# Kernel tuning notes

Hardware: AMD Instinct MI355X
Metric: run time of the kernel (lower is better)

The kernel has to match this reference:

```python
import jax, jax.numpy as jnp
import numpy as np

EPS = 1e-12  # matches torch F.normalize eps

def l2norm(x):
    n = jnp.linalg.norm(x, axis=-1, keepdims=True)
    return x / jnp.maximum(n, EPS)

def setup_inputs() -> dict:
    key = jax.random.key(0)
    ks = jax.random.split(key, 5)
    B, T, A, D, H = 32, 512, 64, 128, 256
    actions = jax.random.normal(ks[0], (B, T, A), dtype=jnp.float32)
    init_structure = jax.random.normal(ks[1], (D,), dtype=jnp.float32)
    # MLP params (scaled like typical init)
    w1 = jax.random.normal(ks[2], (A, H), dtype=jnp.float32) / jnp.sqrt(A)
    b1 = jnp.zeros((H,), dtype=jnp.float32)
    w2 = jax.random.normal(ks[3], (H, D * D), dtype=jnp.float32) / jnp.sqrt(H)
    b2 = jnp.zeros((D * D,), dtype=jnp.float32)
    return {"actions": actions, "init_structure": init_structure,
            "w1": w1, "b1": b1, "w2": w2, "b2": b2}

def reference(actions, init_structure, w1, b1, w2, b2):
    B, T, A = actions.shape
    D = init_structure.shape[0]
    # MLP: actions -> transition matrices [B, T, D, D]
    h = jax.nn.relu(jnp.einsum('bta,ah->bth', actions, w1) + b1)
    trans = (jnp.einsum('bth,hk->btk', h, w2) + b2).reshape(B, T, D, D)
    # initial structure, l2-normalized and broadcast over batch
    s0 = jnp.broadcast_to(l2norm(init_structure), (B, D))
    # sequential recurrence over time
    def step(s, Tm):  # s: [B, D], Tm: [B, D, D]
        s = jax.nn.relu(jnp.einsum('bi,bij->bj', s, Tm))
        s = l2norm(s)
        return s, s
    _, ys = jax.lax.scan(step, s0, jnp.swapaxes(trans, 0, 1))  # ys: [T, B, D]
    return jnp.swapaxes(ys, 0, 1)  # [B, T, D]
```

## Files before the change

kernel.cpp:

```cpp
#include <hip/hip_runtime.h>
#include <stdint.h>
#include <math.h>


typedef _Float16 f16x8 __attribute__((ext_vector_type(8)));
typedef float    f32x4 __attribute__((ext_vector_type(4)));

#define B_  32
#define T_  512
#define A_  64
#define H_  256
#define D_  128
#define N_  (D_ * D_)
#define M_  (B_ * T_)

__device__ inline void glds(const void* g, void* l) {
  __builtin_amdgcn_global_load_lds(
      (__attribute__((address_space(1))) void*)g,
      (__attribute__((address_space(3))) void*)l, 16, 0, 0);
}

__global__ __launch_bounds__(256) void w2cast_kernel(const float* __restrict__ w2,
                                                     _Float16* __restrict__ w2t) {
  __shared__ float tile[64][65];
  const int t = threadIdx.x;
  const int n0 = blockIdx.x * 64, k0 = blockIdx.y * 64;
  const int nn = t & 63, kg = t >> 6;
  #pragma unroll
  for (int r = 0; r < 16; ++r) {
    int k = kg * 16 + r;
    tile[k][nn] = w2[(size_t)(k0 + k) * N_ + n0 + nn];
  }
  __syncthreads();
  const int kk = t & 63, ng = t >> 6;
  #pragma unroll
  for (int r = 0; r < 16; ++r) {
    int n = ng * 16 + r;
    int ngl = n0 + n;
    int i = ngl >> 7, j = ngl & 127;
    int p = ((j >> 4) << 11) | ((i >> 5) << 9) | (((i >> 3) & 3) << 7)
          | ((j & 15) << 3) | (i & 7);
    w2t[(size_t)p * H_ + k0 + kk] = (_Float16)tile[kk][n];
  }
}

__global__ __launch_bounds__(256) void h_kernel(const float* __restrict__ actions,
                                                const float* __restrict__ w1,
                                                const float* __restrict__ b1,
                                                _Float16* __restrict__ h16) {
  __shared__ float w1s[32 * 256];
  __shared__ float acts[32 * 64];
  const int t = threadIdx.x;
  const size_t row0 = (size_t)blockIdx.x * 32;

  #pragma unroll
  for (int i = 0; i < 8; ++i) acts[t + i * 256] = actions[row0 * A_ + t + i * 256];

  float acc[32];
  float bj = b1[t];
  #pragma unroll
  for (int r = 0; r < 32; ++r) acc[r] = bj;

  for (int half = 0; half < 2; ++half) {
    __syncthreads();
    #pragma unroll
    for (int i = 0; i < 32; ++i) w1s[t + i * 256] = w1[half * 32 * 256 + t + i * 256];
    __syncthreads();
    #pragma unroll
    for (int r = 0; r < 32; ++r) {
      float a = acc[r];
      #pragma unroll
      for (int k = 0; k < 32; ++k)
        a += acts[r * 64 + half * 32 + k] * w1s[k * 256 + t];
      acc[r] = a;
    }
  }
  #pragma unroll
  for (int r = 0; r < 32; ++r)
    h16[(row0 + r) * H_ + t] = (_Float16)fmaxf(acc[r], 0.f);
}

__global__ __launch_bounds__(512, 2) void fused_kernel(
    const _Float16* __restrict__ h16, const _Float16* __restrict__ w2t,
    const float* __restrict__ b2, _Float16* __restrict__ tbuf0,
    _Float16* __restrict__ tbuf1, const float* __restrict__ init_s,
    float* __restrict__ out, float* __restrict__ dummyws,
    int Tc, int tcs, int c, int nch) {

  __shared__ __align__(16) char smem[49920];
  const int tid  = threadIdx.x;
  const int lane = tid & 63;
  const int w    = tid >> 6;

  if (blockIdx.x < 32) {
    if (c < 0) return;
    const char* trans = (const char*)((c & 1) ? tbuf1 : tbuf0);
    const int b  = blockIdx.x;
    const int t0 = c * Tc;
    const int n16 = lane & 15, q = lane >> 4;
    const int col = w * 16 + n16;
    float* red = (float*)(smem + 49664);
    _Float16* sb0p = (_Float16*)(smem + 49152);

    float v0 = 0.f;
    if (tid < 128) {
      v0 = (t0 == 0) ? init_s[tid] : out[((size_t)b * T_ + t0 - 1) * D_ + tid];
      float ss = v0 * v0;
      #pragma unroll
      for (int off = 32; off > 0; off >>= 1) ss += __shfl_xor(ss, off);
      if (lane == 0) red[w] = ss;
    }
    __syncthreads();
    if (tid < 128) {
      float inv0 = 1.f / fmaxf(sqrtf(red[0] + red[1]), 1e-12f);
      sb0p[tid] = (_Float16)(v0 * inv0);
    }
    __syncthreads();

    float uprev = (float)sb0p[col];

    const unsigned sbase = (unsigned)(size_t)(__attribute__((address_space(3))) char*)smem;
    const unsigned bq0 = sbase + w * 6144 + q * 256 + n16 * 16;
    const unsigned bq1 = bq0 + 3072;
    const unsigned aA0 = sbase + 49152 + q * 16;
    const unsigned aA1 = aA0 + 256;
    const unsigned aW0 = sbase + 49408 + col * 2;
    const unsigned aW1 = sbase + 49152 + col * 2;
    const char* Gw = trans + (size_t)b * Tc * 32768 + w * 4096 + lane * 16;
    float* outb = out + (size_t)b * T_ * D_ + col;
    float* dsink = dummyws + blockIdx.x * 128 + col;

    f16x8 r3[2];
    {
      const char* g0 = Gw;
      glds(g0,        smem + w * 6144);
      glds(g0 + 1024, smem + w * 6144 + 1024);
      glds(g0 + 2048, smem + w * 6144 + 2048);
      asm volatile("global_load_dwordx4 %0, %1, off"
                   : "=v"(r3[0]) : "v"(g0 + 3072) : "memory");
      const char* g1 = Gw + 32768;
      glds(g1,        smem + w * 6144 + 3072);
      glds(g1 + 1024, smem + w * 6144 + 3072 + 1024);
      glds(g1 + 2048, smem + w * 6144 + 3072 + 2048);
      asm volatile("global_load_dwordx4 %0, %1, off"
                   : "=v"(r3[1]) : "v"(g1 + 3072) : "memory");
    }

    const f32x4 zf = {0.f, 0.f, 0.f, 0.f};

#define STEP(TT, PAR, WAITN)                                                  \
    {                                                                         \
      const int tt = (TT);                                                    \
      f16x8 A0, A1, A2, A3, Bq0, Bq1, Bq2;                                    \
      asm volatile(                                                           \
        "s_waitcnt vmcnt(" #WAITN ")\n\t"                                     \
        "ds_read_b128 %0, %8 offset:0\n\t"                                    \
        "ds_read_b128 %1, %8 offset:64\n\t"                                   \
        "ds_read_b128 %2, %8 offset:128\n\t"                                  \
        "ds_read_b128 %3, %8 offset:192\n\t"                                  \
        "ds_read_b128 %4, %9 offset:0\n\t"                                    \
        "ds_read_b128 %5, %9 offset:1024\n\t"                                 \
        "ds_read_b128 %6, %9 offset:2048\n\t"                                 \
        "s_waitcnt lgkmcnt(0)"                                                \
        : "=v"(A0), "=v"(A1), "=v"(A2), "=v"(A3),                             \
          "=v"(Bq0), "=v"(Bq1), "=v"(Bq2), "+v"(r3[PAR])                      \
        : "v"(aA##PAR), "v"(bq##PAR) : "memory");                             \
      f32x4 c0 = __builtin_amdgcn_mfma_f32_16x16x32_f16(A0, Bq0, zf, 0, 0, 0);\
      f32x4 c1 = __builtin_amdgcn_mfma_f32_16x16x32_f16(A1, Bq1, zf, 0, 0, 0);\
      f32x4 c2 = __builtin_amdgcn_mfma_f32_16x16x32_f16(A2, Bq2, zf, 0, 0, 0);\
      f32x4 c3 = __builtin_amdgcn_mfma_f32_16x16x32_f16(A3, r3[PAR], zf, 0, 0, 0);\
      f32x4 cs = __builtin_amdgcn_mfma_f32_16x16x32_f16(A0, A0, zf, 0, 0, 0); \
      cs = __builtin_amdgcn_mfma_f32_16x16x32_f16(A1, A1, cs, 0, 0, 0);       \
      cs = __builtin_amdgcn_mfma_f32_16x16x32_f16(A2, A2, cs, 0, 0, 0);       \
      cs = __builtin_amdgcn_mfma_f32_16x16x32_f16(A3, A3, cs, 0, 0, 0);       \
      int nt = tt + 2; if (nt >= Tc) nt -= Tc;                                \
      const char* gd = Gw + (size_t)nt * 32768;                               \
      glds(gd,        smem + w * 6144 + (PAR) * 3072);                        \
      glds(gd + 1024, smem + w * 6144 + (PAR) * 3072 + 1024);                 \
      glds(gd + 2048, smem + w * 6144 + (PAR) * 3072 + 2048);                 \
      asm volatile("global_load_dwordx4 %0, %1, off"                          \
                   : "=v"(r3[PAR]) : "v"(gd + 3072) : "memory");              \
      float ssp = cs[0];                                                      \
      float inv = 1.f / fmaxf(sqrtf(ssp), 1e-12f);                            \
      float y = c0[0] + c1[0] + c2[0] + c3[0];                                \
      float un = fmaxf(y, 0.f) * inv;                                         \
      float o = uprev * inv;                                                  \
      uprev = un;                                                             \
      _Float16 hv = (_Float16)un;                                             \
      const int gt = t0 + tt;                                                 \
      float* gp = (gt > 0) ? (outb + (size_t)(gt - 1) * D_) : dsink;          \
      asm volatile("ds_write_b16 %0, %1\n\t"                                  \
                   "global_store_dword %2, %3, off"                           \
                   :: "v"(aW##PAR), "v"(hv), "v"(gp), "v"(o) : "memory");     \
      asm volatile("s_waitcnt lgkmcnt(0)\n\ts_barrier" ::: "memory");         \
    }

    STEP(0, 0, 4)
    STEP(1, 1, 5)
    for (int tt0 = 2; tt0 < Tc; tt0 += 2) {
      STEP(tt0, 0, 6)
      STEP(tt0 + 1, 1, 6)
    }
#undef STEP
    asm volatile("s_waitcnt vmcnt(0)" ::: "memory");

    {
      float x = 0.f;
      if (lane < 16) x = (float)((_Float16*)(smem + 49152))[col];
      float ss2 = x * x;
      ss2 += __shfl_xor(ss2, 1);
      ss2 += __shfl_xor(ss2, 2);
      ss2 += __shfl_xor(ss2, 4);
      ss2 += __shfl_xor(ss2, 8);
      if (lane == 0) red[w] = ss2;
      __syncthreads();
      float tot = 0.f;
      #pragma unroll
      for (int g = 0; g < 8; ++g) tot += red[g];
      float inv = 1.f / fmaxf(sqrtf(tot), 1e-12f);
      if (lane < 16) outb[(size_t)(t0 + Tc - 1) * D_] = uprev * inv;
    }
  } else {
    const int g = c + 1;
    if (g >= nch) return;
    _Float16* trans = (g & 1) ? tbuf1 : tbuf0;
    const int t0g = g * Tc;

    _Float16* smA = (_Float16*)smem;
    _Float16* smB = (_Float16*)(smem + 16384);

    const int wm = w >> 2, wn = w & 3;
    const int fm = lane & 15, fq = lane >> 4;
    const f32x4 zero = {0.f, 0.f, 0.f, 0.f};

    const int cA0 = tid, cA1 = tid + 512;
    const int rA0 = cA0 >> 2, kA0 = cA0 & 3;
    const int rA1 = cA1 >> 2, kA1 = cA1 & 3;

    const int mtiles = (B_ * Tc) >> 8;
    const int ntot = mtiles * 64;
    for (int tile = (int)blockIdx.x - 32; tile < ntot; tile += 224) {
      const int bn = tile & 63;
      const int bm = tile >> 6;

      const int mc0 = bm * 256 + rA0, mc1 = bm * 256 + rA1;
      const int bb0 = mc0 >> tcs, bb1 = mc1 >> tcs;
      const _Float16* gA0 = h16 + ((size_t)bb0 * T_ + t0g + (mc0 & (Tc - 1))) * H_ + kA0 * 8;
      const _Float16* gA1 = h16 + ((size_t)bb1 * T_ + t0g + (mc1 & (Tc - 1))) * H_ + kA1 * 8;
      const _Float16* gB0 = w2t + ((size_t)bn * 256 + rA0) * H_ + kA0 * 8;
      const _Float16* gB1 = w2t + ((size_t)bn * 256 + rA1) * H_ + kA1 * 8;
      _Float16* lA0 = &smA[cA0 * 8];
      _Float16* lA1 = &smA[cA1 * 8];
      _Float16* lB0 = &smB[cA0 * 8];
      _Float16* lB1 = &smB[cA1 * 8];

      f32x4 acc[8][4];
      #pragma unroll
      for (int i = 0; i < 8; ++i)
        #pragma unroll
        for (int j = 0; j < 4; ++j) acc[i][j] = zero;

      for (int kt = 0; kt < H_ / 32; ++kt) {
        __syncthreads();
        glds(gA0 + kt * 32, lA0);
        glds(gA1 + kt * 32, lA1);
        glds(gB0 + kt * 32, lB0);
        glds(gB1 + kt * 32, lB1);
        __syncthreads();
        f16x8 af[8], bf[4];
        #pragma unroll
        for (int mt = 0; mt < 8; ++mt)
          af[mt] = *(const f16x8*)&smA[(wm * 128 + mt * 16 + fm) * 32 + fq * 8];
        #pragma unroll
        for (int nt = 0; nt < 4; ++nt)
          bf[nt] = *(const f16x8*)&smB[(wn * 64 + nt * 16 + fm) * 32 + fq * 8];
        #pragma unroll
        for (int mt = 0; mt < 8; ++mt)
          #pragma unroll
          for (int nt = 0; nt < 4; ++nt)
            acc[mt][nt] = __builtin_amdgcn_mfma_f32_16x16x32_f16(af[mt], bf[nt], acc[mt][nt], 0, 0, 0);
      }

      #pragma unroll
      for (int nt = 0; nt < 4; ++nt) {
        int col = bn * 256 + wn * 64 + nt * 16 + fm;
        int pw = col >> 11, pf = (col >> 9) & 3, pq = (col >> 7) & 3;
        int pn = (col >> 3) & 15, pr = col & 7;
        int ii = pf * 32 + pq * 8 + pr, jj = pw * 16 + pn;
        float bias = b2[ii * 128 + jj];
        #pragma unroll
        for (int mt = 0; mt < 8; ++mt) {
          #pragma unroll
          for (int r = 0; r < 4; ++r) {
            long row = bm * 256 + wm * 128 + mt * 16 + fq * 4 + r;
            trans[row * (long)N_ + col] = (_Float16)(acc[mt][nt][r] + bias);
          }
        }
      }
      __syncthreads();
    }
  }
}

extern "C" void kernel_launch(void* const* d_in, const int* in_sizes, int n_in,
                              void* d_out, int out_size, void* d_ws, size_t ws_size,
                              hipStream_t stream) {
  const float* actions = (const float*)d_in[0];
  const float* init_s  = (const float*)d_in[1];
  const float* w1      = (const float*)d_in[2];
  const float* b1      = (const float*)d_in[3];
  const float* w2      = (const float*)d_in[4];
  const float* b2      = (const float*)d_in[5];
  float* out = (float*)d_out;

  uint8_t* ws = (uint8_t*)d_ws;
  _Float16* w2t = (_Float16*)ws;
  _Float16* h16 = (_Float16*)(ws + ((size_t)8 << 20));
  const size_t trans_off = (size_t)16 << 20;

  int Tc = 16;
  const int cands[3] = {64, 32, 16};
  for (int i = 0; i < 3; ++i) {
    if (trans_off + 2 * ((size_t)cands[i] << 20) + 65536 <= ws_size) { Tc = cands[i]; break; }
  }
  const int tcs = __builtin_ctz(Tc);
  _Float16* tbuf0 = (_Float16*)(ws + trans_off);
  _Float16* tbuf1 = (_Float16*)(ws + trans_off + ((size_t)Tc << 20));
  float* dummyws = (float*)(ws + trans_off + 2 * ((size_t)Tc << 20));

  w2cast_kernel<<<dim3(N_ / 64, 4), 256, 0, stream>>>(w2, w2t);
  h_kernel<<<M_ / 32, 256, 0, stream>>>(actions, w1, b1, h16);

  const int nch = T_ / Tc;
  for (int c = -1; c < nch; ++c) {
    fused_kernel<<<256, 512, 0, stream>>>(
        h16, w2t, b2, tbuf0, tbuf1, init_s, out, dummyws, Tc, tcs, c, nch);
  }
}
```

Measured before the change: 524.2 us.

## Stream transition tiles into a 4-deep register ring instead of LDS

The recurrence blocks now load each step's transition-matrix B fragments straight into registers with four global_load_dwordx4 per slot, keeping a ring four steps deep. Before, three of the four fragments went through LDS via global_load_lds in a two-deep buffer. This removes LDS staging and the ds_reads of B, lengthens prefetch distance to hide global latency, and shrinks shared memory. In exchange it uses many more VGPRs (16 f16x8 ring registers), which could spill under launch_bounds(512,2). The wraparound index now uses a mask, so Tc must be a power of two.

After: 522.7 us. Within noise of the previous version (-0.3%).

```diff
diff --git a/kernel.cpp b/kernel.cpp
--- a/kernel.cpp
+++ b/kernel.cpp
@@ -87,7 +87,7 @@
     float* __restrict__ out, float* __restrict__ dummyws,
     int Tc, int tcs, int c, int nch) {
 
-  __shared__ __align__(16) char smem[49920];
+  __shared__ __align__(16) char smem[33536];
   const int tid  = threadIdx.x;
   const int lane = tid & 63;
   const int w    = tid >> 6;
@@ -99,8 +99,9 @@
     const int t0 = c * Tc;
     const int n16 = lane & 15, q = lane >> 4;
     const int col = w * 16 + n16;
-    float* red = (float*)(smem + 49664);
-    _Float16* sb0p = (_Float16*)(smem + 49152);
+    const int Tcm1 = Tc - 1;
+    float* red = (float*)(smem + 33280);
+    _Float16* sb0p = (_Float16*)(smem + 32768);
 
     float v0 = 0.f;
     if (tid < 128) {
@@ -120,66 +121,55 @@
     float uprev = (float)sb0p[col];
 
     const unsigned sbase = (unsigned)(size_t)(__attribute__((address_space(3))) char*)smem;
-    const unsigned bq0 = sbase + w * 6144 + q * 256 + n16 * 16;
-    const unsigned bq1 = bq0 + 3072;
-    const unsigned aA0 = sbase + 49152 + q * 16;
-    const unsigned aA1 = aA0 + 256;
-    const unsigned aW0 = sbase + 49408 + col * 2;
-    const unsigned aW1 = sbase + 49152 + col * 2;
+    const unsigned aA0 = sbase + 32768 + q * 16;
+    const unsigned aA1 = sbase + 33024 + q * 16;
+    const unsigned aW0 = sbase + 33024 + col * 2;
+    const unsigned aW1 = sbase + 32768 + col * 2;
     const char* Gw = trans + (size_t)b * Tc * 32768 + w * 4096 + lane * 16;
     float* outb = out + (size_t)b * T_ * D_ + col;
     float* dsink = dummyws + blockIdx.x * 128 + col;
 
-    f16x8 r3[2];
-    {
-      const char* g0 = Gw;
-      glds(g0,        smem + w * 6144);
-      glds(g0 + 1024, smem + w * 6144 + 1024);
-      glds(g0 + 2048, smem + w * 6144 + 2048);
-      asm volatile("global_load_dwordx4 %0, %1, off"
-                   : "=v"(r3[0]) : "v"(g0 + 3072) : "memory");
-      const char* g1 = Gw + 32768;
-      glds(g1,        smem + w * 6144 + 3072);
-      glds(g1 + 1024, smem + w * 6144 + 3072 + 1024);
-      glds(g1 + 2048, smem + w * 6144 + 3072 + 2048);
-      asm volatile("global_load_dwordx4 %0, %1, off"
-                   : "=v"(r3[1]) : "v"(g1 + 3072) : "memory");
-    }
+    f16x8 ring[4][4];
+#define LDSLOT(S, P)                                                          \
+    asm volatile("global_load_dwordx4 %0, %4, off\n\t"                        \
+                 "global_load_dwordx4 %1, %4, off offset:1024\n\t"            \
+                 "global_load_dwordx4 %2, %4, off offset:2048\n\t"            \
+                 "global_load_dwordx4 %3, %4, off offset:3072"                \
+                 : "=v"(ring[S][0]), "=v"(ring[S][1]),                        \
+                   "=v"(ring[S][2]), "=v"(ring[S][3])                         \
+                 : "v"(P) : "memory")
+    LDSLOT(0, Gw + 0 * 32768);
+    LDSLOT(1, Gw + 1 * 32768);
+    LDSLOT(2, Gw + 2 * 32768);
+    LDSLOT(3, Gw + 3 * 32768);
 
     const f32x4 zf = {0.f, 0.f, 0.f, 0.f};
 
-#define STEP(TT, PAR, WAITN)                                                  \
+#define STEP(TT, PAR, SPAR, WAITN)                                            \
     {                                                                         \
       const int tt = (TT);                                                    \
-      f16x8 A0, A1, A2, A3, Bq0, Bq1, Bq2;                                    \
+      f16x8 A0, A1, A2, A3;                                                   \
       asm volatile(                                                           \
         "s_waitcnt vmcnt(" #WAITN ")\n\t"                                     \
         "ds_read_b128 %0, %8 offset:0\n\t"                                    \
         "ds_read_b128 %1, %8 offset:64\n\t"                                   \
         "ds_read_b128 %2, %8 offset:128\n\t"                                  \
         "ds_read_b128 %3, %8 offset:192\n\t"                                  \
-        "ds_read_b128 %4, %9 offset:0\n\t"                                    \
-        "ds_read_b128 %5, %9 offset:1024\n\t"                                 \
-        "ds_read_b128 %6, %9 offset:2048\n\t"                                 \
         "s_waitcnt lgkmcnt(0)"                                                \
         : "=v"(A0), "=v"(A1), "=v"(A2), "=v"(A3),                             \
-          "=v"(Bq0), "=v"(Bq1), "=v"(Bq2), "+v"(r3[PAR])                      \
-        : "v"(aA##PAR), "v"(bq##PAR) : "memory");                             \
-      f32x4 c0 = __builtin_amdgcn_mfma_f32_16x16x32_f16(A0, Bq0, zf, 0, 0, 0);\
-      f32x4 c1 = __builtin_amdgcn_mfma_f32_16x16x32_f16(A1, Bq1, zf, 0, 0, 0);\
-      f32x4 c2 = __builtin_amdgcn_mfma_f32_16x16x32_f16(A2, Bq2, zf, 0, 0, 0);\
-      f32x4 c3 = __builtin_amdgcn_mfma_f32_16x16x32_f16(A3, r3[PAR], zf, 0, 0, 0);\
+          "+v"(ring[PAR][0]), "+v"(ring[PAR][1]),                             \
+          "+v"(ring[PAR][2]), "+v"(ring[PAR][3])                              \
+        : "v"(aA##SPAR) : "memory");                                          \
+      f32x4 c0 = __builtin_amdgcn_mfma_f32_16x16x32_f16(A0, ring[PAR][0], zf, 0, 0, 0); \
+      f32x4 c1 = __builtin_amdgcn_mfma_f32_16x16x32_f16(A1, ring[PAR][1], zf, 0, 0, 0); \
+      f32x4 c2 = __builtin_amdgcn_mfma_f32_16x16x32_f16(A2, ring[PAR][2], zf, 0, 0, 0); \
+      f32x4 c3 = __builtin_amdgcn_mfma_f32_16x16x32_f16(A3, ring[PAR][3], zf, 0, 0, 0); \
       f32x4 cs = __builtin_amdgcn_mfma_f32_16x16x32_f16(A0, A0, zf, 0, 0, 0); \
       cs = __builtin_amdgcn_mfma_f32_16x16x32_f16(A1, A1, cs, 0, 0, 0);       \
       cs = __builtin_amdgcn_mfma_f32_16x16x32_f16(A2, A2, cs, 0, 0, 0);       \
       cs = __builtin_amdgcn_mfma_f32_16x16x32_f16(A3, A3, cs, 0, 0, 0);       \
-      int nt = tt + 2; if (nt >= Tc) nt -= Tc;                                \
-      const char* gd = Gw + (size_t)nt * 32768;                               \
-      glds(gd,        smem + w * 6144 + (PAR) * 3072);                        \
-      glds(gd + 1024, smem + w * 6144 + (PAR) * 3072 + 1024);                 \
-      glds(gd + 2048, smem + w * 6144 + (PAR) * 3072 + 2048);                 \
-      asm volatile("global_load_dwordx4 %0, %1, off"                          \
-                   : "=v"(r3[PAR]) : "v"(gd + 3072) : "memory");              \
+      const char* gd = Gw + (size_t)((tt + 4) & Tcm1) * 32768;                \
+      LDSLOT(PAR, gd);                                                        \
       float ssp = cs[0];                                                      \
       float inv = 1.f / fmaxf(sqrtf(ssp), 1e-12f);                            \
       float y = c0[0] + c1[0] + c2[0] + c3[0];                                \
@@ -191,22 +181,27 @@
       float* gp = (gt > 0) ? (outb + (size_t)(gt - 1) * D_) : dsink;          \
       asm volatile("ds_write_b16 %0, %1\n\t"                                  \
                    "global_store_dword %2, %3, off"                           \
-                   :: "v"(aW##PAR), "v"(hv), "v"(gp), "v"(o) : "memory");     \
+                   :: "v"(aW##SPAR), "v"(hv), "v"(gp), "v"(o) : "memory");    \
       asm volatile("s_waitcnt lgkmcnt(0)\n\ts_barrier" ::: "memory");         \
     }
 
-    STEP(0, 0, 4)
-    STEP(1, 1, 5)
-    for (int tt0 = 2; tt0 < Tc; tt0 += 2) {
-      STEP(tt0, 0, 6)
-      STEP(tt0 + 1, 1, 6)
+    STEP(0, 0, 0, 12)
+    STEP(1, 1, 1, 13)
+    STEP(2, 2, 0, 14)
+    STEP(3, 3, 1, 15)
+    for (int tt0 = 4; tt0 < Tc; tt0 += 4) {
+      STEP(tt0,     0, 0, 16)
+      STEP(tt0 + 1, 1, 1, 16)
+      STEP(tt0 + 2, 2, 0, 16)
+      STEP(tt0 + 3, 3, 1, 16)
     }
 #undef STEP
+#undef LDSLOT
     asm volatile("s_waitcnt vmcnt(0)" ::: "memory");
 
     {
       float x = 0.f;
-      if (lane < 16) x = (float)((_Float16*)(smem + 49152))[col];
+      if (lane < 16) x = (float)((_Float16*)(smem + 32768))[col];
       float ss2 = x * x;
       ss2 += __shfl_xor(ss2, 1);
       ss2 += __shfl_xor(ss2, 2);
```
